# Performance work log

Measured on AMD Instinct MI355X. Metric: run time of the kernel, lower is better.

The kernel has to match this reference:

```python
import jax, jax.numpy as jnp
import numpy as np
import math

B, S, D, H = 4, 1024, 1024, 16
DH = D // H  # 64
NEG = -100000000000.0


def setup_inputs() -> dict:
    key = jax.random.key(0)
    ks = jax.random.split(key, 9)
    sc_in = 1.0 / math.sqrt(D)
    sc_h = 1.0 / math.sqrt(DH)
    return {
        "x": jax.random.normal(ks[0], (B, S, D), dtype=jnp.float32),
        # per-head projection weights stacked over the head axis [H, D, DH]
        "Wq": jax.random.normal(ks[1], (H, D, DH), dtype=jnp.float32) * sc_in,
        "bq": jnp.zeros((H, DH), dtype=jnp.float32),
        "Wk": jax.random.normal(ks[2], (H, D, DH), dtype=jnp.float32) * sc_in,
        "bk": jnp.zeros((H, DH), dtype=jnp.float32),
        "Wv": jax.random.normal(ks[3], (H, D, DH), dtype=jnp.float32) * sc_in,
        "bv": jnp.zeros((H, DH), dtype=jnp.float32),
        # output feed-forward: Dense(D, gelu) applied to the [B,S,DH] head-sum
        "Wf": jax.random.normal(ks[4], (DH, D), dtype=jnp.float32) * sc_h,
        "bf": jnp.zeros((D,), dtype=jnp.float32),
    }


def reference(x, Wq, bq, Wk, bk, Wv, bv, Wf, bf):
    # per-head q,k,v: [B,H,S,DH]
    q = jnp.einsum('bsd,hde->bhse', x, Wq) + bq[None, :, None, :]
    k = jnp.einsum('bsd,hde->bhse', x, Wk) + bk[None, :, None, :]
    v = jnp.einsum('bsd,hde->bhse', x, Wv) + bv[None, :, None, :]
    scale = 1.0 / math.sqrt(DH)
    # causal mask as in source: triu(ones, 1) * -1e11 added to scores
    mask = jnp.triu(jnp.ones((S, S), dtype=jnp.float32), 1) * NEG
    scores = jnp.einsum('bhse,bhte->bhst', q, k) * scale + mask  # [B,H,S,S]
    w = jax.nn.softmax(scores, axis=-1)
    z = jnp.einsum('bhst,bhte->bhse', w, v)  # [B,H,S,DH]
    # faithful to source bug: heads are SUMMED, not concatenated
    summed = jnp.sum(z, axis=1)  # [B,S,DH]
    # ff Dense with exact (erf) gelu, keras tf.nn.gelu default approximate=False
    out = jax.nn.gelu(summed @ Wf + bf, approximate=False)  # [B,S,D]
    # dropout is identity at inference
    return out
```

## Files before the change

kernel.cpp:

```cpp
#include <hip/hip_runtime.h>
#include <hip/hip_bf16.h>
#include <math.h>

#define BB 4
#define SS 1024
#define DD 1024
#define HH 16
#define DH 64

#define GM 4096
#define GN 3072
#define GK 1024

typedef __attribute__((ext_vector_type(4))) float f32x4;
typedef __attribute__((ext_vector_type(8))) short bf16x8;

__device__ __forceinline__ unsigned int pack2bf(float a, float b) {
    __hip_bfloat16 x = __float2bfloat16(a), y = __float2bfloat16(b);
    return (unsigned int)__builtin_bit_cast(unsigned short, x) |
           ((unsigned int)__builtin_bit_cast(unsigned short, y) << 16);
}

__device__ __forceinline__ int swz8(int row) { return (row ^ (row >> 2)) & 7; }

__global__ __launch_bounds__(256) void convert_x(const float* __restrict__ x,
                                                 __hip_bfloat16* __restrict__ xb)
{
    int i = (blockIdx.x * 256 + threadIdx.x) * 4;
    float4 xv = *(const float4*)(x + i);
    xb[i + 0] = __float2bfloat16(xv.x);
    xb[i + 1] = __float2bfloat16(xv.y);
    xb[i + 2] = __float2bfloat16(xv.z);
    xb[i + 3] = __float2bfloat16(xv.w);
}

__global__ __launch_bounds__(256) void wt_kernel(
    const float* __restrict__ Wq, const float* __restrict__ Wk,
    const float* __restrict__ Wv, __hip_bfloat16* __restrict__ WbT)
{
    const int z = blockIdx.y >> 4;
    const int h = blockIdx.y & 15;
    const int d0 = blockIdx.x * 64;
    const int tid = threadIdx.x;
    const float* W = (z == 0) ? Wq : (z == 1) ? Wk : Wv;
    const float* src = W + (size_t)h * DD * DH;

    __shared__ float tile[64][65];

    #pragma unroll
    for (int p = 0; p < 16; p++) {
        int d = p * 4 + (tid >> 6);
        int e = tid & 63;
        tile[d][e] = src[(size_t)(d0 + d) * DH + e];
    }
    __syncthreads();
    #pragma unroll
    for (int p = 0; p < 16; p++) {
        int e = p * 4 + (tid >> 6);
        int d = tid & 63;
        WbT[(size_t)(z * 1024 + h * 64 + e) * GK + d0 + d] =
            __float2bfloat16(tile[d][e]);
    }
}

__global__ __launch_bounds__(256) void gemm_qkv(
    const unsigned short* __restrict__ A,
    const unsigned short* __restrict__ Bt,
    const float* __restrict__ bq, const float* __restrict__ bk,
    const float* __restrict__ bv,
    unsigned short* __restrict__ q, unsigned short* __restrict__ k,
    unsigned short* __restrict__ v)
{
    __shared__ unsigned short As[128 * 64];
    __shared__ unsigned short Bs[128 * 64];

    const int tid  = threadIdx.x;
    const int wave = tid >> 6;
    const int lane = tid & 63;
    const int m0 = blockIdx.x * 128;
    const int n0 = blockIdx.y * 128;
    const int wy = wave >> 1, wx = wave & 1;
    const bool vblk = (n0 >= 2048);

    f32x4 acc[4][4];
    #pragma unroll
    for (int i = 0; i < 4; i++)
        #pragma unroll
        for (int j = 0; j < 4; j++)
            acc[i][j] = (f32x4){0.f, 0.f, 0.f, 0.f};

    const int srow0 = (wave * 4) * 8;
    const int lrow  = lane >> 3;
    const int lcs   = lane & 7;

    for (int ko = 0; ko < GK; ko += 64) {
        __syncthreads();
        #pragma unroll
        for (int c = 0; c < 4; c++) {
            int row = srow0 + c * 8 + lrow;
            int chunk = lcs ^ (row & 7);
            const unsigned short* ga = A + (size_t)(m0 + row) * GK + ko + chunk * 8;
            const unsigned short* gb = Bt + (size_t)(n0 + row) * GK + ko + chunk * 8;
            unsigned short* la = As + ((size_t)(wave * 4 + c) * 64) * 8;
            unsigned short* lb = Bs + ((size_t)(wave * 4 + c) * 64) * 8;
            __builtin_amdgcn_global_load_lds(
                (const __attribute__((address_space(1))) unsigned int*)ga,
                (__attribute__((address_space(3))) unsigned int*)la, 16, 0, 0);
            __builtin_amdgcn_global_load_lds(
                (const __attribute__((address_space(1))) unsigned int*)gb,
                (__attribute__((address_space(3))) unsigned int*)lb, 16, 0, 0);
        }
        __syncthreads();

        const int mrow = lane & 15;
        const int quad = lane >> 4;
        #pragma unroll
        for (int ks = 0; ks < 2; ks++) {
            bf16x8 af[4], bfr[4];
            #pragma unroll
            for (int mt = 0; mt < 4; mt++) {
                int row = wy * 64 + mt * 16 + mrow;
                int chunk = (ks * 4 + quad) ^ (row & 7);
                af[mt] = *(const bf16x8*)(As + row * 64 + chunk * 8);
            }
            #pragma unroll
            for (int nt = 0; nt < 4; nt++) {
                int row = wx * 64 + nt * 16 + mrow;
                int chunk = (ks * 4 + quad) ^ (row & 7);
                bfr[nt] = *(const bf16x8*)(Bs + row * 64 + chunk * 8);
            }
            if (vblk) {
                #pragma unroll
                for (int mt = 0; mt < 4; mt++)
                    #pragma unroll
                    for (int nt = 0; nt < 4; nt++)
                        acc[mt][nt] = __builtin_amdgcn_mfma_f32_16x16x32_bf16(
                            af[mt], bfr[nt], acc[mt][nt], 0, 0, 0);
            } else {
                #pragma unroll
                for (int nt = 0; nt < 4; nt++)
                    #pragma unroll
                    for (int mt = 0; mt < 4; mt++)
                        acc[nt][mt] = __builtin_amdgcn_mfma_f32_16x16x32_bf16(
                            bfr[nt], af[mt], acc[nt][mt], 0, 0, 0);
            }
        }
    }

    const int quad = lane >> 4;
    const int cl   = lane & 15;
    const int h    = ((n0 + wx * 64) >> 6) & 15;

    if (!vblk) {
        const int z = n0 >> 10;
        const float* bias = (z == 0) ? bq : bk;
        unsigned short* outp = (z == 0) ? q : k;
        const float sc = (z == 0) ? 0.125f : 1.0f;
        #pragma unroll
        for (int nt = 0; nt < 4; nt++) {
            int ebase = nt * 16 + quad * 4;
            float4 b4 = *(const float4*)(bias + h * 64 + ebase);
            #pragma unroll
            for (int mt = 0; mt < 4; mt++) {
                int m = m0 + wy * 64 + mt * 16 + cl;
                int b = m >> 10, s = m & 1023;
                f32x4 a = acc[nt][mt];
                float v0 = (a[0] + b4.x) * sc;
                float v1 = (a[1] + b4.y) * sc;
                float v2 = (a[2] + b4.z) * sc;
                float v3 = (a[3] + b4.w) * sc;
                uint2 pk = make_uint2(pack2bf(v0, v1), pack2bf(v2, v3));
                *(uint2*)(outp + ((size_t)((b * 16 + h) * 1024 + s)) * 64 + ebase) = pk;
            }
        }
    } else {
        #pragma unroll
        for (int nt = 0; nt < 4; nt++) {
            int e = nt * 16 + cl;
            float bb = bv[h * 64 + e];
            #pragma unroll
            for (int mt = 0; mt < 4; mt++) {
                int rbase = m0 + wy * 64 + mt * 16 + quad * 4;
                int b = rbase >> 10, s = rbase & 1023;
                f32x4 a = acc[mt][nt];
                uint2 pk = make_uint2(pack2bf(a[0] + bb, a[1] + bb),
                                      pack2bf(a[2] + bb, a[3] + bb));
                *(uint2*)(v + ((size_t)((b * 16 + h) * 64 + e)) * 1024 + s) = pk;
            }
        }
    }
}

__global__ __launch_bounds__(256) void flash_attn(
    const unsigned short* __restrict__ qg, const unsigned short* __restrict__ kg,
    const unsigned short* __restrict__ vtg, float* __restrict__ summed)
{
    __shared__ unsigned short Qs[4096];
    __shared__ unsigned short Ks[2][4096];
    __shared__ unsigned short Vts[2][4096];

    const int x  = blockIdx.x;
    const int y  = blockIdx.y;
    const int qi = (x + (y & 15) + ((y >> 4) << 2)) & 15;
    const int q0 = qi * 64;
    const int bh = y;
    const int b  = bh >> 4;
    const int tid  = threadIdx.x;
    const int wave = tid >> 6;
    const int lane = tid & 63;
    const int lrow = lane >> 3;
    const int lcs  = lane & 7;
    const int m16  = lane & 15;
    const int quad = lane >> 4;

    const unsigned short* qb = qg + (size_t)bh * SS * DH;
    const unsigned short* kb = kg + (size_t)bh * SS * DH;
    const unsigned short* vb = vtg + (size_t)bh * SS * DH;

    #pragma unroll
    for (int c = 0; c < 2; c++) {
        int region = wave * 2 + c;
        int row = region * 8 + lrow;
        int g = lcs ^ swz8(row);
        __builtin_amdgcn_global_load_lds(
            (const __attribute__((address_space(1))) unsigned int*)
                (qb + (size_t)(q0 + row) * DH + g * 8),
            (__attribute__((address_space(3))) unsigned int*)(Qs + region * 512),
            16, 0, 0);
        __builtin_amdgcn_global_load_lds(
            (const __attribute__((address_space(1))) unsigned int*)
                (kb + (size_t)row * DH + g * 8),
            (__attribute__((address_space(3))) unsigned int*)(&Ks[0][region * 512]),
            16, 0, 0);
        __builtin_amdgcn_global_load_lds(
            (const __attribute__((address_space(1))) unsigned int*)
                (vb + (size_t)row * SS + g * 8),
            (__attribute__((address_space(3))) unsigned int*)(&Vts[0][region * 512]),
            16, 0, 0);
    }

    f32x4 accO[4];
    float lsum = 0.f;
    #pragma unroll
    for (int nt = 0; nt < 4; nt++) accO[nt] = (f32x4){0.f, 0.f, 0.f, 0.f};

    bf16x8 af0, af1;
    const int rloc = wave * 16 + m16;

    for (int tt = 0; tt <= qi; tt++) {
        __syncthreads();

        if (tt == 0) {
            int row = wave * 16 + m16;
            af0 = *(const bf16x8*)(Qs + row * 64 + ((quad ^ swz8(row)) * 8));
            af1 = *(const bf16x8*)(Qs + row * 64 + (((4 + quad) ^ swz8(row)) * 8));
        }

        if (tt < qi) {
            const int t1 = (tt + 1) * 64;
            const int bn = (tt + 1) & 1;
            #pragma unroll
            for (int c = 0; c < 2; c++) {
                int region = wave * 2 + c;
                int row = region * 8 + lrow;
                int g = lcs ^ swz8(row);
                __builtin_amdgcn_global_load_lds(
                    (const __attribute__((address_space(1))) unsigned int*)
                        (kb + (size_t)(t1 + row) * DH + g * 8),
                    (__attribute__((address_space(3))) unsigned int*)
                        (&Ks[bn][region * 512]), 16, 0, 0);
                __builtin_amdgcn_global_load_lds(
                    (const __attribute__((address_space(1))) unsigned int*)
                        (vb + (size_t)row * SS + t1 + g * 8),
                    (__attribute__((address_space(3))) unsigned int*)
                        (&Vts[bn][region * 512]), 16, 0, 0);
            }
        }

        const unsigned short* uK = &Ks[tt & 1][0];
        const unsigned short* uV = &Vts[tt & 1][0];

        f32x4 acc[4];
        #pragma unroll
        for (int nt = 0; nt < 4; nt++) {
            int row = ((nt & 2) << 4) + ((m16 >> 2) << 3) + ((nt & 1) << 2) + (m16 & 3);
            bf16x8 kf0 = *(const bf16x8*)(uK + row * 64 + ((quad ^ swz8(row)) * 8));
            bf16x8 kf1 = *(const bf16x8*)(uK + row * 64 + (((4 + quad) ^ swz8(row)) * 8));
            f32x4 a = (f32x4){0.f, 0.f, 0.f, 0.f};
            a = __builtin_amdgcn_mfma_f32_16x16x32_bf16(kf0, af0, a, 0, 0, 0);
            a = __builtin_amdgcn_mfma_f32_16x16x32_bf16(kf1, af1, a, 0, 0, 0);
            acc[nt] = a;
        }

        const bool diag = (tt == qi);
        bf16x8 pf0, pf1;
        #pragma unroll
        for (int nt = 0; nt < 4; nt++) {
            #pragma unroll
            for (int r = 0; r < 4; r++) {
                int tl = ((nt & 2) << 4) + (quad << 3) + ((nt & 1) << 2) + r;
                float s = acc[nt][r];
                if (diag && tl > rloc) s = -1e30f;
                float p = __expf(s);
                lsum += p;
                __hip_bfloat16 hb = __float2bfloat16(p);
                short pb = (short)__builtin_bit_cast(unsigned short, hb);
                int j = ((nt & 1) << 2) + r;
                if (nt < 2) pf0[j] = pb; else pf1[j] = pb;
            }
        }

        #pragma unroll
        for (int nt = 0; nt < 4; nt++) {
            int row = nt * 16 + m16;
            bf16x8 vf0 = *(const bf16x8*)(uV + row * 64 + ((quad ^ swz8(row)) * 8));
            bf16x8 vf1 = *(const bf16x8*)(uV + row * 64 + (((4 + quad) ^ swz8(row)) * 8));
            accO[nt] = __builtin_amdgcn_mfma_f32_16x16x32_bf16(vf0, pf0, accO[nt],
                                                               0, 0, 0);
            accO[nt] = __builtin_amdgcn_mfma_f32_16x16x32_bf16(vf1, pf1, accO[nt],
                                                               0, 0, 0);
        }
    }

    float l = lsum;
    l += __shfl_xor(l, 16);
    l += __shfl_xor(l, 32);
    const float invl = 1.f / l;

    __syncthreads();
    float* buf = (wave < 2) ? (float*)&Ks[0][0] : (float*)&Vts[0][0];
    buf += (wave & 1) * (16 * 66);
    #pragma unroll
    for (int nt = 0; nt < 4; nt++) {
        f32x4 w4 = accO[nt];
        w4 *= invl;
        *(f32x4*)(buf + m16 * 66 + nt * 16 + quad * 4) = w4;
    }
    __asm__ volatile("s_waitcnt lgkmcnt(0)" ::: "memory");

    float* dstbase = summed + ((size_t)b * SS + q0 + wave * 16) * DH;
    #pragma unroll
    for (int rr = 0; rr < 16; rr++) {
        float valr = buf[rr * 66 + lane];
        atomicAdd(dstbase + (size_t)rr * DH + lane, valr);
    }
}

__global__ __launch_bounds__(256) void ff_kernel(
    const float* __restrict__ summed, const float* __restrict__ Wf,
    const float* __restrict__ bf, float* __restrict__ out)
{
    const int r   = blockIdx.x;
    const int tid = threadIdx.x;
    __shared__ float sm[DH];
    if (tid < DH) sm[tid] = summed[(size_t)r * DH + tid];
    __syncthreads();

    for (int d = tid; d < DD; d += 256) {
        float acc = bf[d];
        #pragma unroll 8
        for (int e = 0; e < DH; e++) acc += sm[e] * Wf[(size_t)e * DD + d];
        out[(size_t)r * DD + d] = 0.5f * acc * (1.f + erff(acc * 0.70710678118654752f));
    }
}

extern "C" void kernel_launch(void* const* d_in, const int* in_sizes, int n_in,
                              void* d_out, int out_size, void* d_ws, size_t ws_size,
                              hipStream_t stream) {
    const float* x  = (const float*)d_in[0];
    const float* Wq = (const float*)d_in[1];
    const float* bq = (const float*)d_in[2];
    const float* Wk = (const float*)d_in[3];
    const float* bk = (const float*)d_in[4];
    const float* Wv = (const float*)d_in[5];
    const float* bv = (const float*)d_in[6];
    const float* Wf = (const float*)d_in[7];
    const float* bf = (const float*)d_in[8];
    float* out = (float*)d_out;

    const size_t per = (size_t)BB * HH * SS * DH;
    unsigned short* q   = (unsigned short*)d_ws;
    unsigned short* k   = q + per;
    unsigned short* v   = k + per;
    float* summed       = (float*)(v + per);
    __hip_bfloat16* xb  = (__hip_bfloat16*)(summed + (size_t)BB * SS * DH);
    __hip_bfloat16* WbT = xb + (size_t)BB * SS * DD;

    hipMemsetAsync(summed, 0, (size_t)BB * SS * DH * sizeof(float), stream);

    convert_x<<<(BB * SS * DD) / (256 * 4), 256, 0, stream>>>(x, xb);
    wt_kernel<<<dim3(DD / 64, 3 * HH), 256, 0, stream>>>(Wq, Wk, Wv, WbT);

    gemm_qkv<<<dim3(GM / 128, GN / 128), 256, 0, stream>>>(
        (const unsigned short*)xb, (const unsigned short*)WbT,
        bq, bk, bv, q, k, v);

    flash_attn<<<dim3(SS / 64, BB * HH), 256, 0, stream>>>(q, k, v, summed);

    ff_kernel<<<BB * SS, 256, 0, stream>>>(summed, Wf, bf, out);
}
```

Before: 203.8 us.

## Replace scalar FF dense with bf16 MFMA GEMM using transposed Wf

Adds a kernel that transposes Wf to bf16 [D, DH] and replaces the per-row scalar FF kernel with a tiled 128x128 MFMA GEMM. That GEMM converts the summed activations to bf16 in LDS and fuses bias and erf-GELU into the epilogue. The old kernel ran one block per row and re-read Wf from global memory for every row with scalar FMAs. The new path lowers precision of the FF input and weights to bf16 and adds one small extra launch.

Measured after the change: 173.9 us. -14.7%, faster.

```diff
diff --git a/kernel.cpp b/kernel.cpp
--- a/kernel.cpp
+++ b/kernel.cpp
@@ -60,6 +60,30 @@
         int d = tid & 63;
         WbT[(size_t)(z * 1024 + h * 64 + e) * GK + d0 + d] =
             __float2bfloat16(tile[d][e]);
+    }
+}
+
+__global__ __launch_bounds__(256) void wft_kernel(
+    const float* __restrict__ Wf, unsigned short* __restrict__ WfT)
+{
+    const int d0 = blockIdx.x * 64;
+    const int tid = threadIdx.x;
+    __shared__ float tile[64][65];
+
+    #pragma unroll
+    for (int p = 0; p < 16; p++) {
+        int e  = p * 4 + (tid >> 6);
+        int dd = tid & 63;
+        tile[e][dd] = Wf[(size_t)e * DD + d0 + dd];
+    }
+    __syncthreads();
+    #pragma unroll
+    for (int p = 0; p < 16; p++) {
+        int dd = p * 4 + (tid >> 6);
+        int e  = tid & 63;
+        __hip_bfloat16 hb = __float2bfloat16(tile[e][dd]);
+        WfT[(size_t)(d0 + dd) * DH + e] =
+            __builtin_bit_cast(unsigned short, hb);
     }
 }
 
@@ -346,21 +370,93 @@
     }
 }
 
-__global__ __launch_bounds__(256) void ff_kernel(
-    const float* __restrict__ summed, const float* __restrict__ Wf,
-    const float* __restrict__ bf, float* __restrict__ out)
-{
-    const int r   = blockIdx.x;
-    const int tid = threadIdx.x;
-    __shared__ float sm[DH];
-    if (tid < DH) sm[tid] = summed[(size_t)r * DH + tid];
+__global__ __launch_bounds__(256) void ff_mfma(
+    const float* __restrict__ summed, const unsigned short* __restrict__ WfT,
+    const float* __restrict__ bfb, float* __restrict__ out)
+{
+    __shared__ unsigned short As[128 * 64];
+    __shared__ unsigned short Bs[128 * 64];
+
+    const int tid  = threadIdx.x;
+    const int wave = tid >> 6;
+    const int lane = tid & 63;
+    const int m0 = blockIdx.x * 128;
+    const int n0 = blockIdx.y * 128;
+    const int wy = wave >> 1, wx = wave & 1;
+    const int lrow = lane >> 3;
+    const int lcs  = lane & 7;
+
+    #pragma unroll
+    for (int c = 0; c < 4; c++) {
+        int row = (wave * 4 + c) * 8 + lrow;
+        int chunk = lcs ^ (row & 7);
+        __builtin_amdgcn_global_load_lds(
+            (const __attribute__((address_space(1))) unsigned int*)
+                (WfT + (size_t)(n0 + row) * DH + chunk * 8),
+            (__attribute__((address_space(3))) unsigned int*)
+                (Bs + ((wave * 4 + c) * 64) * 8), 16, 0, 0);
+    }
+    #pragma unroll
+    for (int i = 0; i < 4; i++) {
+        int chunkid = tid + i * 256;
+        int row = chunkid >> 3, c = chunkid & 7;
+        const float* src = summed + (size_t)(m0 + row) * DH + c * 8;
+        float4 a = *(const float4*)src;
+        float4 bq = *(const float4*)(src + 4);
+        uint4 pk;
+        pk.x = pack2bf(a.x, a.y);  pk.y = pack2bf(a.z, a.w);
+        pk.z = pack2bf(bq.x, bq.y); pk.w = pack2bf(bq.z, bq.w);
+        *(uint4*)(As + row * 64 + ((c ^ (row & 7)) * 8)) = pk;
+    }
     __syncthreads();
 
-    for (int d = tid; d < DD; d += 256) {
-        float acc = bf[d];
-        #pragma unroll 8
-        for (int e = 0; e < DH; e++) acc += sm[e] * Wf[(size_t)e * DD + d];
-        out[(size_t)r * DD + d] = 0.5f * acc * (1.f + erff(acc * 0.70710678118654752f));
+    f32x4 acc[4][4];
+    #pragma unroll
+    for (int i = 0; i < 4; i++)
+        #pragma unroll
+        for (int j = 0; j < 4; j++)
+            acc[i][j] = (f32x4){0.f, 0.f, 0.f, 0.f};
+
+    const int mrow = lane & 15;
+    const int quad = lane >> 4;
+    #pragma unroll
+    for (int ks = 0; ks < 2; ks++) {
+        bf16x8 af[4], bfr[4];
+        #pragma unroll
+        for (int mt = 0; mt < 4; mt++) {
+            int row = wy * 64 + mt * 16 + mrow;
+            int chunk = (ks * 4 + quad) ^ (row & 7);
+            af[mt] = *(const bf16x8*)(As + row * 64 + chunk * 8);
+        }
+        #pragma unroll
+        for (int nt = 0; nt < 4; nt++) {
+            int row = wx * 64 + nt * 16 + mrow;
+            int chunk = (ks * 4 + quad) ^ (row & 7);
+            bfr[nt] = *(const bf16x8*)(Bs + row * 64 + chunk * 8);
+        }
+        #pragma unroll
+        for (int mt = 0; mt < 4; mt++)
+            #pragma unroll
+            for (int nt = 0; nt < 4; nt++)
+                acc[mt][nt] = __builtin_amdgcn_mfma_f32_16x16x32_bf16(
+                    af[mt], bfr[nt], acc[mt][nt], 0, 0, 0);
+    }
+
+    const int cl = lane & 15;
+    #pragma unroll
+    for (int nt = 0; nt < 4; nt++) {
+        int d = n0 + wx * 64 + nt * 16 + cl;
+        float bb = bfb[d];
+        #pragma unroll
+        for (int mt = 0; mt < 4; mt++) {
+            int rbase = m0 + wy * 64 + mt * 16 + quad * 4;
+            #pragma unroll
+            for (int r = 0; r < 4; r++) {
+                float vA = acc[mt][nt][r] + bb;
+                out[(size_t)(rbase + r) * DD + d] =
+                    0.5f * vA * (1.f + erff(vA * 0.70710678118654752f));
+            }
+        }
     }
 }
 
@@ -385,11 +481,13 @@
     float* summed       = (float*)(v + per);
     __hip_bfloat16* xb  = (__hip_bfloat16*)(summed + (size_t)BB * SS * DH);
     __hip_bfloat16* WbT = xb + (size_t)BB * SS * DD;
+    unsigned short* WfT = (unsigned short*)(WbT + (size_t)GN * GK);
 
     hipMemsetAsync(summed, 0, (size_t)BB * SS * DH * sizeof(float), stream);
 
     convert_x<<<(BB * SS * DD) / (256 * 4), 256, 0, stream>>>(x, xb);
     wt_kernel<<<dim3(DD / 64, 3 * HH), 256, 0, stream>>>(Wq, Wk, Wv, WbT);
+    wft_kernel<<<DD / 64, 256, 0, stream>>>(Wf, WfT);
 
     gemm_qkv<<<dim3(GM / 128, GN / 128), 256, 0, stream>>>(
         (const unsigned short*)xb, (const unsigned short*)WbT,
@@ -397,5 +495,5 @@
 
     flash_attn<<<dim3(SS / 64, BB * HH), 256, 0, stream>>>(q, k, v, summed);
 
-    ff_kernel<<<BB * SS, 256, 0, stream>>>(summed, Wf, bf, out);
-}
+    ff_mfma<<<dim3(GM / 128, DD / 128), 256, 0, stream>>>(summed, WfT, bf, out);
+}
```
